# Performance work log

Measured on AMD Instinct MI355X. Metric: run time of the kernel, lower is better.

The kernel has to match this reference:

```python
import jax, jax.numpy as jnp
import numpy as np

NUM_ITERATIONS = 3


def squash(s, axis=-1):
    # v = (|s|^2 / (1+|s|^2)) * s / |s|  (standard CapsNet squash)
    sq_norm = jnp.sum(s * s, axis=axis, keepdims=True)
    return (sq_norm / (1.0 + sq_norm)) * s / jnp.sqrt(sq_norm + 1e-9)


def setup_inputs() -> dict:
    key = jax.random.key(0)
    k1, k2 = jax.random.split(key)
    B, IN_C, OUT_C, OUT_D, IN_D = 64, 2048, 32, 16, 8
    x = jax.random.normal(k1, (B, IN_C, IN_D), dtype=jnp.float32)
    W = jax.random.normal(k2, (1, IN_C, OUT_C, OUT_D, IN_D), dtype=jnp.float32)
    return {"x": x, "W": W}


def reference(x, W):
    # u_hat[b,i,o,d] = sum_m W[0,i,o,d,m] * x[b,i,m]
    u_hat = jnp.einsum('iodm,bim->biod', W[0], x)  # [B, IN_C, OUT_C, OUT_D]
    B, IN_C, OUT_C, _ = u_hat.shape
    b_logits = jnp.zeros((B, IN_C, OUT_C), dtype=u_hat.dtype)
    v = None
    for _ in range(NUM_ITERATIONS):
        # PyTorch F.softmax(b) with implicit dim=1 for a 4-D tensor -> softmax over in_channels
        c = jax.nn.softmax(b_logits, axis=1)               # [B, IN_C, OUT_C]
        s = jnp.einsum('bio,biod->bod', c, u_hat)          # [B, OUT_C, OUT_D]
        v = squash(s)                                      # [B, OUT_C, OUT_D]
        b_logits = b_logits + jnp.einsum('biod,bod->bio', u_hat, v)
    return v
```

## Files before the change

### kernel.cpp

```cpp
#include <hip/hip_runtime.h>
#include <math.h>

#define B_ 64
#define IC 2048
#define OC 32
#define OD 16
#define ID 8

typedef __attribute__((ext_vector_type(8)))  short s16x8;
typedef __attribute__((ext_vector_type(16))) float f32x16;

#define GLOAD_LDS16(gp, lp)                                                       \
  __builtin_amdgcn_global_load_lds((const __attribute__((address_space(1))) void*)(gp), \
                                   (__attribute__((address_space(3))) void*)(lp), \
                                   16, 0, 0)

__device__ __forceinline__ unsigned short f2bf(float f) {
  unsigned u = __float_as_uint(f);
  return (unsigned short)((u + 0x7fffu + ((u >> 16) & 1u)) >> 16);
}
__device__ __forceinline__ float bf2f(unsigned short h) {
  return __uint_as_float(((unsigned)h) << 16);
}
__device__ __forceinline__ f32x16 mfma16(s16x8 a, s16x8 b, f32x16 c) {
  return __builtin_amdgcn_mfma_f32_32x32x16_bf16(a, b, c, 0, 0, 0);
}
__device__ __forceinline__ float dot8(const float4 w0, const float4 w1,
                                      const float4 xa, const float4 xb) {
  return w0.x*xa.x + w0.y*xa.y + w0.z*xa.z + w0.w*xa.w
       + w1.x*xb.x + w1.y*xb.y + w1.z*xb.z + w1.w*xb.w;
}

__global__ __launch_bounds__(256) void convWX(
    const float* __restrict__ W, const float* __restrict__ x,
    unsigned short* __restrict__ Wbf, unsigned short* __restrict__ xb)
{
  const int bid = blockIdx.x;
  if (bid < 8192) {
    const int e4 = bid * 256 + threadIdx.x;
    const float4 v = ((const float4*)W)[e4];
    const int i = e4 >> 10;
    const int r = (e4 & 1023) << 2;
    ushort4 h, l;
    h.x = f2bf(v.x); l.x = f2bf(v.x - bf2f(h.x));
    h.y = f2bf(v.y); l.y = f2bf(v.y - bf2f(h.y));
    h.z = f2bf(v.z); l.z = f2bf(v.z - bf2f(h.z));
    h.w = f2bf(v.w); l.w = f2bf(v.w - bf2f(h.w));
    *(ushort4*)&Wbf[(size_t)i * 8192 + r]        = h;
    *(ushort4*)&Wbf[(size_t)i * 8192 + 4096 + r] = l;
  } else {
    const int idx = (bid - 8192) * 256 + threadIdx.x;
    const int m2 = idx & 1, i = (idx >> 1) & 2047, b = idx >> 12;
    const float4 v = *(const float4*)(x + (size_t)b * 16384 + i * 8 + m2 * 4);
    ushort4 h, l;
    h.x = f2bf(v.x); l.x = f2bf(v.x - bf2f(h.x));
    h.y = f2bf(v.y); l.y = f2bf(v.y - bf2f(h.y));
    h.z = f2bf(v.z); l.z = f2bf(v.z - bf2f(h.z));
    h.w = f2bf(v.w); l.w = f2bf(v.w - bf2f(h.w));
    *(ushort4*)&xb[(size_t)i * 1024 + b * 8 + m2 * 4]       = h;
    *(ushort4*)&xb[(size_t)i * 1024 + 512 + b * 8 + m2 * 4] = l;
  }
}

template<bool WEIGHTED, int NCH>
__global__ __launch_bounds__(256) void fusedM(
    const unsigned short* __restrict__ Wbf, const unsigned short* __restrict__ xb,
    const float* __restrict__ vss, float* __restrict__ part,
    float* __restrict__ zpart)
{
  constexpr int CI = IC / NCH;
  const int t     = threadIdx.x;
  const int ch    = blockIdx.x % NCH;
  const int q     = blockIdx.x / NCH;
  const int lane  = t & 63;
  const int wv    = t >> 6;
  const int s     = q * 4 + wv;
  const int opair = s >> 1;
  const int bt    = s & 1;
  const int l31   = lane & 31;
  const int hb    = lane >> 5;
  const int i0    = ch * CI;

  const unsigned short* ap =
      Wbf + (size_t)i0 * 8192 + opair * 256 + (l31 >> 4) * 128 + (lane & 15) * 8;
  const unsigned short* bp =
      xb + (size_t)i0 * 1024 + hb * 512 + bt * 256 + l31 * 8;

  f32x16 acc = (f32x16)0.0f;
  float zA = 0.f, zB = 0.f;
  float vsr[16];

  if constexpr (WEIGHTED) {
    const float* vp = vss + s * 1024 + hb * 32 + l31;
#pragma unroll
    for (int r = 0; r < 16; ++r) vsr[r] = vp[r * 64];
  }

  s16x8 AH[3], AL[3], BV[3];
  AH[0] = *(const s16x8*)ap;
  AL[0] = *(const s16x8*)(ap + 4096);
  BV[0] = *(const s16x8*)bp;
  if (CI > 1) {
    AH[1] = *(const s16x8*)(ap + 8192);
    AL[1] = *(const s16x8*)(ap + 8192 + 4096);
    BV[1] = *(const s16x8*)(bp + 1024);
  }

#pragma unroll
  for (int ii = 0; ii < CI; ++ii) {
    const int cs = ii % 3;
    const int ns = (ii + 2) % 3;
    if (ii + 2 < CI) {
      AH[ns] = *(const s16x8*)(ap + (size_t)(ii + 2) * 8192);
      AL[ns] = *(const s16x8*)(ap + (size_t)(ii + 2) * 8192 + 4096);
      BV[ns] = *(const s16x8*)(bp + (size_t)(ii + 2) * 1024);
    }

    if constexpr (!WEIGHTED) {
      acc = mfma16(AH[cs], BV[cs], acc);
      acc = mfma16(AL[cs], BV[cs], acc);
    } else {
      f32x16 u = mfma16(AH[cs], BV[cs], (f32x16)0.0f);
      u = mfma16(AL[cs], BV[cs], u);
      float pdA = 0.f, pdB = 0.f;
#pragma unroll
      for (int r = 0; r < 8; ++r)  pdA = fmaf(u[r], vsr[r], pdA);
#pragma unroll
      for (int r = 8; r < 16; ++r) pdB = fmaf(u[r], vsr[r], pdB);
      pdA += __shfl_xor(pdA, 32);
      pdB += __shfl_xor(pdB, 32);
      const float pA = __expf(pdA), pB = __expf(pdB);
#pragma unroll
      for (int r = 0; r < 8; ++r)  acc[r] = fmaf(pA, u[r], acc[r]);
#pragma unroll
      for (int r = 8; r < 16; ++r) acc[r] = fmaf(pB, u[r], acc[r]);
      zA += pA; zB += pB;
    }
  }

  float* op = part + (size_t)ch * 32768;
#pragma unroll
  for (int r = 0; r < 16; ++r)
    op[(s * 16 + r) * 64 + hb * 32 + l31] = acc[r];
  if constexpr (WEIGHTED) {
    if (lane < 32) {
      zpart[(size_t)ch * 2048 + (s * 2 + 0) * 32 + lane] = zA;
      zpart[(size_t)ch * 2048 + (s * 2 + 1) * 32 + lane] = zB;
    }
  }
}

template<int PASS, int NCH>
__global__ __launch_bounds__(512) void rsqM(
    const float* __restrict__ part, const float* __restrict__ zpart,
    float* __restrict__ vss, float* __restrict__ out)
{
  __shared__ float rzs[32];
  __shared__ float sqs[512];
  const int t   = threadIdx.x;
  const int blk = blockIdx.x;
  const int s   = blk >> 1, oo = blk & 1;
  const int l31 = t & 31, hb = (t >> 5) & 1, rr = t >> 6;
  const size_t tid = (size_t)blk * 512 + t;

  float acc = 0.f;
#pragma unroll 8
  for (int ch = 0; ch < NCH; ++ch) acc += part[(size_t)ch * 32768 + tid];

  if constexpr (PASS == 0) {
    if (t < 32) rzs[t] = 1.f / 2048.f;
  } else {
    if (t < 32) {
      float zs = 0.f;
#pragma unroll 8
      for (int ch = 0; ch < NCH; ++ch)
        zs += zpart[(size_t)ch * 2048 + (s * 2 + oo) * 32 + t];
      rzs[t] = 1.f / zs;
    }
  }
  __syncthreads();
  const float sv = acc * rzs[l31];
  sqs[t] = sv * sv;
  __syncthreads();
  float sq = 0.f;
#pragma unroll
  for (int k = 0; k < 16; ++k) sq += sqs[l31 + k * 32];
  const float f = (sq / (1.f + sq)) * rsqrtf(sq + 1e-9f);
  const float v = sv * f;

  if constexpr (PASS == 0)      vss[tid] = v;
  else if constexpr (PASS == 1) vss[tid] += v;
  else {
    const int b = (s & 1) * 32 + l31;
    const int o = (s >> 1) * 2 + oo;
    const int d = (rr & 3) + 8 * (rr >> 2) + 4 * hb;
    out[(b * 32 + o) * 16 + d] = v;
  }
}

template<bool WEIGHTED, int NCH>
__global__ __launch_bounds__(512) void fusedF32(
    const float* __restrict__ x, const float* __restrict__ W,
    const float* __restrict__ vs, float* __restrict__ part,
    float* __restrict__ zpart)
{
  constexpr int CI  = IC / NCH;
  constexpr int NSW = CI / 8;
  const int t    = threadIdx.x;
  const int xcd  = blockIdx.x & 7;
  const int q    = blockIdx.x >> 3;
  const int ch   = (q >> 2) * 8 + xcd;
  const int bh   = q & 3;
  const int lane = t & 63;
  const int wv   = t >> 6;
  const int og   = wv >> 2;
  const int bset = wv & 3;
  const int op   = lane >> 2;
  const int dq   = lane & 3;
  const int o    = og * 16 + op;
  const int rot  = lane & 7;
  const int i0   = ch * CI;
  const int jb   = o * 32 + dq * 8;
  const int bl0  = bset * 4;
  const int b0   = bh * 16 + bl0;

  __shared__ float Wbuf[2][4096];
  __shared__ float xall[1024];

  const float4* Wg = (const float4*)W;
  const float4* xg = (const float4*)x;

  float4 acc[4];
  float  zacc[4];
  float4 vreg[4];
#pragma unroll
  for (int k = 0; k < 4; ++k) { acc[k] = make_float4(0,0,0,0); zacc[k] = 0.f; }

  if constexpr (WEIGHTED) {
#pragma unroll
    for (int bb = 0; bb < 4; ++bb)
      vreg[bb] = *(const float4*)(vs + ((size_t)(b0 + bb) * 32 + o) * 16 + dq * 4);
  }

  auto stageW = [&](int i, int nb) {
    const float4* Wi = Wg + (size_t)i * 1024;
#pragma unroll
    for (int k = 0; k < 2; ++k) {
      const int p   = wv * 128 + k * 64 + lane;
      const int src = (p & ~7) | ((p & 7) ^ ((p >> 3) & 7));
      GLOAD_LDS16(Wi + src, &Wbuf[nb][(wv * 128 + k * 64) * 4]);
    }
  };
  auto stageX = [&](int sw) {
    if (t < 256) {
      const int b = t >> 4, r = t & 15;
      const int ia = i0 + sw * 8 + (r >> 1);
      GLOAD_LDS16(xg + ((size_t)(bh * 16 + b) * IC + ia) * 2 + (r & 1),
                  &xall[(wv * 64) * 4]);
    }
  };

  stageX(0);
  stageW(i0, 0);
  int cur = 0;

#pragma unroll 1
  for (int sw = 0; sw < NSW; ++sw) {
#pragma unroll 1
    for (int j = 0; j < 8; ++j) {
      const int ii = sw * 8 + j;
      __syncthreads();
      if (ii + 1 < CI) stageW(i0 + ii + 1, cur ^ 1);

      const float* Wb = &Wbuf[cur][0];
      float4 wr[8];
#pragma unroll
      for (int r = 0; r < 8; ++r)
        wr[r] = *(const float4*)&Wb[(jb + (r ^ rot)) * 4];

#pragma unroll
      for (int bb = 0; bb < 4; ++bb) {
        const int bl = bl0 + bb;
        const float4 xa = *(const float4*)&xall[bl * 64 + j * 8];
        const float4 xc = *(const float4*)&xall[bl * 64 + j * 8 + 4];
        float4 u;
        u.x = dot8(wr[0], wr[1], xa, xc);
        u.y = dot8(wr[2], wr[3], xa, xc);
        u.z = dot8(wr[4], wr[5], xa, xc);
        u.w = dot8(wr[6], wr[7], xa, xc);
        if constexpr (!WEIGHTED) {
          acc[bb].x += u.x; acc[bb].y += u.y; acc[bb].z += u.z; acc[bb].w += u.w;
        } else {
          const float4 vv = vreg[bb];
          float pd = u.x * vv.x + u.y * vv.y + u.z * vv.z + u.w * vv.w;
          pd += __shfl_xor(pd, 1);
          pd += __shfl_xor(pd, 2);
          const float p = __expf(pd);
          acc[bb].x = fmaf(p, u.x, acc[bb].x);
          acc[bb].y = fmaf(p, u.y, acc[bb].y);
          acc[bb].z = fmaf(p, u.z, acc[bb].z);
          acc[bb].w = fmaf(p, u.w, acc[bb].w);
          zacc[bb] += p;
        }
      }
      cur ^= 1;
    }
    if (sw + 1 < NSW) { __syncthreads(); stageX(sw + 1); }
  }

  float4* part4 = (float4*)part;
#pragma unroll
  for (int bb = 0; bb < 4; ++bb) {
    const int b = b0 + bb;
    part4[((size_t)ch * 64 + b) * 128 + o * 4 + dq] = acc[bb];
    if constexpr (WEIGHTED) {
      if (dq == 0) zpart[(size_t)ch * 2048 + b * 32 + o] = zacc[bb];
    }
  }
}

template<int PASS, int NCH>
__global__ __launch_bounds__(256) void reduceSquash(
    const float* __restrict__ part, const float* __restrict__ rz,
    float* __restrict__ vsio, float* __restrict__ out)
{
  const int g = blockIdx.x * 256 + threadIdx.x;
  float s = 0.f;
#pragma unroll 8
  for (int ch = 0; ch < NCH; ++ch) s += part[(size_t)ch * 32768 + g];
  if constexpr (PASS == 0) s *= (1.f / 2048.f);
  else                     s *= rz[g >> 4];

  float sq = s * s;
#pragma unroll
  for (int k = 1; k < 16; k <<= 1) sq += __shfl_xor(sq, k);
  const float f = (sq / (1.f + sq)) * rsqrtf(sq + 1e-9f);
  const float v = s * f;

  if constexpr (PASS == 0)      vsio[g] = v;
  else if constexpr (PASS == 1) vsio[g] += v;
  else                          out[g] = v;
}

template<int NCH>
__global__ __launch_bounds__(256) void zredK(
    const float* __restrict__ zpart, float* __restrict__ rz)
{
  const int j = blockIdx.x * 256 + threadIdx.x;
  float zs = 0.f;
#pragma unroll 8
  for (int ch = 0; ch < NCH; ++ch) zs += zpart[(size_t)ch * 2048 + j];
  rz[j] = 1.f / zs;
}

extern "C" void kernel_launch(void* const* d_in, const int* in_sizes, int n_in,
                              void* d_out, int out_size, void* d_ws, size_t ws_size,
                              hipStream_t stream) {
  (void)in_sizes; (void)n_in; (void)out_size;
  const float* x = (const float*)d_in[0];
  const float* W = (const float*)d_in[1];
  float* out = (float*)d_out;
  float* ws  = (float*)d_ws;

  const size_t WBF_US = (size_t)IC * 8192;
  const size_t XB_US  = (size_t)IC * 1024;

  auto runM = [&](auto tag) {
    constexpr int NCH = decltype(tag)::value;
    float* part  = ws;
    float* zpart = part + (size_t)NCH * 32768;
    float* vsb   = zpart + (size_t)NCH * 2048;
    unsigned short* Wbf = (unsigned short*)(vsb + 32768);
    unsigned short* xbp = Wbf + WBF_US;

    const dim3 b256(256), b512(512), gF(8 * NCH), gR(64);
    convWX<<<dim3(9216), b256, 0, stream>>>(W, x, Wbf, xbp);
    fusedM<false, NCH><<<gF, b256, 0, stream>>>(Wbf, xbp, nullptr, part, nullptr);
    rsqM<0, NCH><<<gR, b512, 0, stream>>>(part, nullptr, vsb, nullptr);
    fusedM<true, NCH><<<gF, b256, 0, stream>>>(Wbf, xbp, vsb, part, zpart);
    rsqM<1, NCH><<<gR, b512, 0, stream>>>(part, zpart, vsb, nullptr);
    fusedM<true, NCH><<<gF, b256, 0, stream>>>(Wbf, xbp, vsb, part, zpart);
    rsqM<2, NCH><<<gR, b512, 0, stream>>>(part, zpart, nullptr, out);
  };

  auto runF = [&](auto tag) {
    constexpr int NCH = decltype(tag)::value;
    float* part  = ws;
    float* zpart = part + (size_t)NCH * 32768;
    float* rz    = zpart + (size_t)NCH * 2048;
    float* vsb   = rz + 2048;

    const dim3 gF(4 * NCH), bF(512), b256(256), gR(128);
    fusedF32<false, NCH><<<gF, bF, 0, stream>>>(x, W, nullptr, part, nullptr);
    reduceSquash<0, NCH><<<gR, b256, 0, stream>>>(part, nullptr, vsb, nullptr);
    fusedF32<true, NCH><<<gF, bF, 0, stream>>>(x, W, vsb, part, zpart);
    zredK<NCH><<<dim3(8), b256, 0, stream>>>(zpart, rz);
    reduceSquash<1, NCH><<<gR, b256, 0, stream>>>(part, rz, vsb, nullptr);
    fusedF32<true, NCH><<<gF, bF, 0, stream>>>(x, W, vsb, part, zpart);
    zredK<NCH><<<dim3(8), b256, 0, stream>>>(zpart, rz);
    reduceSquash<2, NCH><<<gR, b256, 0, stream>>>(part, rz, nullptr, out);
  };

  auto needM = [&](size_t nch) -> size_t {
    return (nch * 32768 + nch * 2048 + 32768) * 4 + (WBF_US + XB_US) * 2;
  };
  const size_t needF256 = ((size_t)256 * 32768 + 256ul * 2048 + 2048 + 32768) * 4;

  if      (ws_size >= needM(128)) runM(std::integral_constant<int, 128>{});
  else if (ws_size >= needM(64))  runM(std::integral_constant<int, 64>{});
  else if (ws_size >= needF256)   runF(std::integral_constant<int, 256>{});
  else                            runF(std::integral_constant<int, 64>{});
}
```

Baseline: 95.35 us.

## Split fused MFMA pass across 256 chunks with two-stage partial reduction

Raises the number of input-channel chunks for the MFMA routing kernel from 128 to 256, doubling the grid of the main compute kernels. The single-stage reduction over chunks is replaced by a two-stage reduction: rsqA sums groups of 16 chunks across 1024 blocks, then rsqB sums the 16 group results and applies the squash. This aims to fill more compute units and to avoid a long serial reduction in a 64-block kernel, at the cost of more partial-sum traffic and an extra launch per iteration. The fp32 fallback path and its kernels are removed.

```diff
diff --git a/kernel.cpp b/kernel.cpp
--- a/kernel.cpp
+++ b/kernel.cpp
@@ -10,11 +10,6 @@
 typedef __attribute__((ext_vector_type(8)))  short s16x8;
 typedef __attribute__((ext_vector_type(16))) float f32x16;
 
-#define GLOAD_LDS16(gp, lp)                                                       \
-  __builtin_amdgcn_global_load_lds((const __attribute__((address_space(1))) void*)(gp), \
-                                   (__attribute__((address_space(3))) void*)(lp), \
-                                   16, 0, 0)
-
 __device__ __forceinline__ unsigned short f2bf(float f) {
   unsigned u = __float_as_uint(f);
   return (unsigned short)((u + 0x7fffu + ((u >> 16) & 1u)) >> 16);
@@ -24,11 +19,6 @@
 }
 __device__ __forceinline__ f32x16 mfma16(s16x8 a, s16x8 b, f32x16 c) {
   return __builtin_amdgcn_mfma_f32_32x32x16_bf16(a, b, c, 0, 0, 0);
-}
-__device__ __forceinline__ float dot8(const float4 w0, const float4 w1,
-                                      const float4 xa, const float4 xb) {
-  return w0.x*xa.x + w0.y*xa.y + w0.z*xa.z + w0.w*xa.w
-       + w1.x*xb.x + w1.y*xb.y + w1.z*xb.z + w1.w*xb.w;
 }
 
 __global__ __launch_bounds__(256) void convWX(
@@ -150,6 +140,86 @@
   }
 }
 
+template<bool WEIGHTED, int NCH>
+__global__ __launch_bounds__(512) void rsqA(
+    const float* __restrict__ part, const float* __restrict__ zpart,
+    float* __restrict__ pp2, float* __restrict__ zp2)
+{
+  constexpr int CPG = NCH / 16;
+  const int t  = threadIdx.x;
+  const int g  = blockIdx.x >> 6;
+  const int sl = blockIdx.x & 63;
+  const size_t tid = (size_t)sl * 512 + t;
+
+  float acc = 0.f;
+#pragma unroll 8
+  for (int c = 0; c < CPG; ++c)
+    acc += part[(size_t)(g * CPG + c) * 32768 + tid];
+  pp2[(size_t)g * 32768 + tid] = acc;
+
+  if constexpr (WEIGHTED) {
+    if (sl == 0) {
+#pragma unroll
+      for (int k = 0; k < 4; ++k) {
+        const int j = t + 512 * k;
+        float zs = 0.f;
+#pragma unroll 8
+        for (int c = 0; c < CPG; ++c)
+          zs += zpart[(size_t)(g * CPG + c) * 2048 + j];
+        zp2[(size_t)g * 2048 + j] = zs;
+      }
+    }
+  }
+}
+
+template<int PASS>
+__global__ __launch_bounds__(512) void rsqB(
+    const float* __restrict__ pp2, const float* __restrict__ zp2,
+    float* __restrict__ vss, float* __restrict__ out)
+{
+  __shared__ float rzs[32];
+  __shared__ float sqs[512];
+  const int t   = threadIdx.x;
+  const int blk = blockIdx.x;
+  const int s   = blk >> 1, oo = blk & 1;
+  const int l31 = t & 31, hb = (t >> 5) & 1, rr = t >> 6;
+  const size_t tid = (size_t)blk * 512 + t;
+
+  float acc = 0.f;
+#pragma unroll
+  for (int g = 0; g < 16; ++g) acc += pp2[(size_t)g * 32768 + tid];
+
+  if constexpr (PASS == 0) {
+    if (t < 32) rzs[t] = 1.f / 2048.f;
+  } else {
+    if (t < 32) {
+      float zs = 0.f;
+#pragma unroll
+      for (int g = 0; g < 16; ++g)
+        zs += zp2[(size_t)g * 2048 + (s * 2 + oo) * 32 + t];
+      rzs[t] = 1.f / zs;
+    }
+  }
+  __syncthreads();
+  const float sv = acc * rzs[l31];
+  sqs[t] = sv * sv;
+  __syncthreads();
+  float sq = 0.f;
+#pragma unroll
+  for (int k = 0; k < 16; ++k) sq += sqs[l31 + k * 32];
+  const float f = (sq / (1.f + sq)) * rsqrtf(sq + 1e-9f);
+  const float v = sv * f;
+
+  if constexpr (PASS == 0)      vss[tid] = v;
+  else if constexpr (PASS == 1) vss[tid] += v;
+  else {
+    const int b = (s & 1) * 32 + l31;
+    const int o = (s >> 1) * 2 + oo;
+    const int d = (rr & 3) + 8 * (rr >> 2) + 4 * hb;
+    out[(b * 32 + o) * 16 + d] = v;
+  }
+}
+
 template<int PASS, int NCH>
 __global__ __launch_bounds__(512) void rsqM(
     const float* __restrict__ part, const float* __restrict__ zpart,
@@ -198,161 +268,6 @@
   }
 }
 
-template<bool WEIGHTED, int NCH>
-__global__ __launch_bounds__(512) void fusedF32(
-    const float* __restrict__ x, const float* __restrict__ W,
-    const float* __restrict__ vs, float* __restrict__ part,
-    float* __restrict__ zpart)
-{
-  constexpr int CI  = IC / NCH;
-  constexpr int NSW = CI / 8;
-  const int t    = threadIdx.x;
-  const int xcd  = blockIdx.x & 7;
-  const int q    = blockIdx.x >> 3;
-  const int ch   = (q >> 2) * 8 + xcd;
-  const int bh   = q & 3;
-  const int lane = t & 63;
-  const int wv   = t >> 6;
-  const int og   = wv >> 2;
-  const int bset = wv & 3;
-  const int op   = lane >> 2;
-  const int dq   = lane & 3;
-  const int o    = og * 16 + op;
-  const int rot  = lane & 7;
-  const int i0   = ch * CI;
-  const int jb   = o * 32 + dq * 8;
-  const int bl0  = bset * 4;
-  const int b0   = bh * 16 + bl0;
-
-  __shared__ float Wbuf[2][4096];
-  __shared__ float xall[1024];
-
-  const float4* Wg = (const float4*)W;
-  const float4* xg = (const float4*)x;
-
-  float4 acc[4];
-  float  zacc[4];
-  float4 vreg[4];
-#pragma unroll
-  for (int k = 0; k < 4; ++k) { acc[k] = make_float4(0,0,0,0); zacc[k] = 0.f; }
-
-  if constexpr (WEIGHTED) {
-#pragma unroll
-    for (int bb = 0; bb < 4; ++bb)
-      vreg[bb] = *(const float4*)(vs + ((size_t)(b0 + bb) * 32 + o) * 16 + dq * 4);
-  }
-
-  auto stageW = [&](int i, int nb) {
-    const float4* Wi = Wg + (size_t)i * 1024;
-#pragma unroll
-    for (int k = 0; k < 2; ++k) {
-      const int p   = wv * 128 + k * 64 + lane;
-      const int src = (p & ~7) | ((p & 7) ^ ((p >> 3) & 7));
-      GLOAD_LDS16(Wi + src, &Wbuf[nb][(wv * 128 + k * 64) * 4]);
-    }
-  };
-  auto stageX = [&](int sw) {
-    if (t < 256) {
-      const int b = t >> 4, r = t & 15;
-      const int ia = i0 + sw * 8 + (r >> 1);
-      GLOAD_LDS16(xg + ((size_t)(bh * 16 + b) * IC + ia) * 2 + (r & 1),
-                  &xall[(wv * 64) * 4]);
-    }
-  };
-
-  stageX(0);
-  stageW(i0, 0);
-  int cur = 0;
-
-#pragma unroll 1
-  for (int sw = 0; sw < NSW; ++sw) {
-#pragma unroll 1
-    for (int j = 0; j < 8; ++j) {
-      const int ii = sw * 8 + j;
-      __syncthreads();
-      if (ii + 1 < CI) stageW(i0 + ii + 1, cur ^ 1);
-
-      const float* Wb = &Wbuf[cur][0];
-      float4 wr[8];
-#pragma unroll
-      for (int r = 0; r < 8; ++r)
-        wr[r] = *(const float4*)&Wb[(jb + (r ^ rot)) * 4];
-
-#pragma unroll
-      for (int bb = 0; bb < 4; ++bb) {
-        const int bl = bl0 + bb;
-        const float4 xa = *(const float4*)&xall[bl * 64 + j * 8];
-        const float4 xc = *(const float4*)&xall[bl * 64 + j * 8 + 4];
-        float4 u;
-        u.x = dot8(wr[0], wr[1], xa, xc);
-        u.y = dot8(wr[2], wr[3], xa, xc);
-        u.z = dot8(wr[4], wr[5], xa, xc);
-        u.w = dot8(wr[6], wr[7], xa, xc);
-        if constexpr (!WEIGHTED) {
-          acc[bb].x += u.x; acc[bb].y += u.y; acc[bb].z += u.z; acc[bb].w += u.w;
-        } else {
-          const float4 vv = vreg[bb];
-          float pd = u.x * vv.x + u.y * vv.y + u.z * vv.z + u.w * vv.w;
-          pd += __shfl_xor(pd, 1);
-          pd += __shfl_xor(pd, 2);
-          const float p = __expf(pd);
-          acc[bb].x = fmaf(p, u.x, acc[bb].x);
-          acc[bb].y = fmaf(p, u.y, acc[bb].y);
-          acc[bb].z = fmaf(p, u.z, acc[bb].z);
-          acc[bb].w = fmaf(p, u.w, acc[bb].w);
-          zacc[bb] += p;
-        }
-      }
-      cur ^= 1;
-    }
-    if (sw + 1 < NSW) { __syncthreads(); stageX(sw + 1); }
-  }
-
-  float4* part4 = (float4*)part;
-#pragma unroll
-  for (int bb = 0; bb < 4; ++bb) {
-    const int b = b0 + bb;
-    part4[((size_t)ch * 64 + b) * 128 + o * 4 + dq] = acc[bb];
-    if constexpr (WEIGHTED) {
-      if (dq == 0) zpart[(size_t)ch * 2048 + b * 32 + o] = zacc[bb];
-    }
-  }
-}
-
-template<int PASS, int NCH>
-__global__ __launch_bounds__(256) void reduceSquash(
-    const float* __restrict__ part, const float* __restrict__ rz,
-    float* __restrict__ vsio, float* __restrict__ out)
-{
-  const int g = blockIdx.x * 256 + threadIdx.x;
-  float s = 0.f;
-#pragma unroll 8
-  for (int ch = 0; ch < NCH; ++ch) s += part[(size_t)ch * 32768 + g];
-  if constexpr (PASS == 0) s *= (1.f / 2048.f);
-  else                     s *= rz[g >> 4];
-
-  float sq = s * s;
-#pragma unroll
-  for (int k = 1; k < 16; k <<= 1) sq += __shfl_xor(sq, k);
-  const float f = (sq / (1.f + sq)) * rsqrtf(sq + 1e-9f);
-  const float v = s * f;
-
-  if constexpr (PASS == 0)      vsio[g] = v;
-  else if constexpr (PASS == 1) vsio[g] += v;
-  else                          out[g] = v;
-}
-
-template<int NCH>
-__global__ __launch_bounds__(256) void zredK(
-    const float* __restrict__ zpart, float* __restrict__ rz)
-{
-  const int j = blockIdx.x * 256 + threadIdx.x;
-  float zs = 0.f;
-#pragma unroll 8
-  for (int ch = 0; ch < NCH; ++ch) zs += zpart[(size_t)ch * 2048 + j];
-  rz[j] = 1.f / zs;
-}
-
 extern "C" void kernel_launch(void* const* d_in, const int* in_sizes, int n_in,
                               void* d_out, int out_size, void* d_ws, size_t ws_size,
                               hipStream_t stream) {
@@ -365,13 +280,44 @@
   const size_t WBF_US = (size_t)IC * 8192;
   const size_t XB_US  = (size_t)IC * 1024;
 
-  auto runM = [&](auto tag) {
-    constexpr int NCH = decltype(tag)::value;
+  const size_t need256 =
+      ((size_t)256 * 32768 + 256ul * 2048 + 16ul * 32768 + 16ul * 2048 + 32768) * 4
+      + (WBF_US + XB_US) * 2;
+  const size_t need128 =
+      ((size_t)128 * 32768 + 128ul * 2048 + 32768) * 4 + (WBF_US + XB_US) * 2;
+
+  if (ws_size >= need256) {
+    constexpr int NCH = 256;
+    float* part  = ws;
+    float* zpart = part + (size_t)NCH * 32768;
+    float* pp2   = zpart + (size_t)NCH * 2048;
+    float* zp2   = pp2 + 16ul * 32768;
+    float* vsb   = zp2 + 16ul * 2048;
+    unsigned short* Wbf = (unsigned short*)(vsb + 32768);
+    unsigned short* xbp = Wbf + WBF_US;
+
+    const dim3 b256(256), b512(512), gF(8 * NCH), gA(1024), gB(64);
+    convWX<<<dim3(9216), b256, 0, stream>>>(W, x, Wbf, xbp);
+    fusedM<false, NCH><<<gF, b256, 0, stream>>>(Wbf, xbp, nullptr, part, nullptr);
+    rsqA<false, NCH><<<gA, b512, 0, stream>>>(part, nullptr, pp2, nullptr);
+    rsqB<0><<<gB, b512, 0, stream>>>(pp2, nullptr, vsb, nullptr);
+    fusedM<true, NCH><<<gF, b256, 0, stream>>>(Wbf, xbp, vsb, part, zpart);
+    rsqA<true, NCH><<<gA, b512, 0, stream>>>(part, zpart, pp2, zp2);
+    rsqB<1><<<gB, b512, 0, stream>>>(pp2, zp2, vsb, nullptr);
+    fusedM<true, NCH><<<gF, b256, 0, stream>>>(Wbf, xbp, vsb, part, zpart);
+    rsqA<true, NCH><<<gA, b512, 0, stream>>>(part, zpart, pp2, zp2);
+    rsqB<2><<<gB, b512, 0, stream>>>(pp2, zp2, nullptr, out);
+    return;
+  }
+
+  {
+    constexpr int NCH = 128;
     float* part  = ws;
     float* zpart = part + (size_t)NCH * 32768;
     float* vsb   = zpart + (size_t)NCH * 2048;
     unsigned short* Wbf = (unsigned short*)(vsb + 32768);
     unsigned short* xbp = Wbf + WBF_US;
+    (void)need128;
 
     const dim3 b256(256), b512(512), gF(8 * NCH), gR(64);
     convWX<<<dim3(9216), b256, 0, stream>>>(W, x, Wbf, xbp);
@@ -381,33 +327,5 @@
     rsqM<1, NCH><<<gR, b512, 0, stream>>>(part, zpart, vsb, nullptr);
     fusedM<true, NCH><<<gF, b256, 0, stream>>>(Wbf, xbp, vsb, part, zpart);
     rsqM<2, NCH><<<gR, b512, 0, stream>>>(part, zpart, nullptr, out);
-  };
-
-  auto runF = [&](auto tag) {
-    constexpr int NCH = decltype(tag)::value;
-    float* part  = ws;
-    float* zpart = part + (size_t)NCH * 32768;
-    float* rz    = zpart + (size_t)NCH * 2048;
-    float* vsb   = rz + 2048;
-
-    const dim3 gF(4 * NCH), bF(512), b256(256), gR(128);
-    fusedF32<false, NCH><<<gF, bF, 0, stream>>>(x, W, nullptr, part, nullptr);
-    reduceSquash<0, NCH><<<gR, b256, 0, stream>>>(part, nullptr, vsb, nullptr);
-    fusedF32<true, NCH><<<gF, bF, 0, stream>>>(x, W, vsb, part, zpart);
-    zredK<NCH><<<dim3(8), b256, 0, stream>>>(zpart, rz);
-    reduceSquash<1, NCH><<<gR, b256, 0, stream>>>(part, rz, vsb, nullptr);
-    fusedF32<true, NCH><<<gF, bF, 0, stream>>>(x, W, vsb, part, zpart);
-    zredK<NCH><<<dim3(8), b256, 0, stream>>>(zpart, rz);
-    reduceSquash<2, NCH><<<gR, b256, 0, stream>>>(part, rz, nullptr, out);
-  };
-
-  auto needM = [&](size_t nch) -> size_t {
-    return (nch * 32768 + nch * 2048 + 32768) * 4 + (WBF_US + XB_US) * 2;
-  };
-  const size_t needF256 = ((size_t)256 * 32768 + 256ul * 2048 + 2048 + 32768) * 4;
-
-  if      (ws_size >= needM(128)) runM(std::integral_constant<int, 128>{});
-  else if (ws_size >= needM(64))  runM(std::integral_constant<int, 64>{});
-  else if (ws_size >= needF256)   runF(std::integral_constant<int, 256>{});
-  else                            runF(std::integral_constant<int, 64>{});
-}
+  }
+}
```

Result: slower. 100.8 us (+5.7%).
